# Performance work log

Hardware: AMD Instinct MI355X
Metric: run time of the kernel (lower is better)

## Reference

```python
import jax, jax.numpy as jnp
import numpy as np
from jax import lax

TOP_K = 6
NORM_MIN = 1e-12


def setup_inputs() -> dict:
    key = jax.random.key(0)
    k0, k1, k2, k3, k4, k5 = jax.random.split(key, 6)
    B, S, H, E, I = 2, 1024, 2048, 64, 512
    return {
        "hidden_states": jax.random.normal(k0, (B, S, H), dtype=jnp.float32),
        "gate_w": jax.random.normal(k1, (E, H), dtype=jnp.float32) * 0.02,
        "e_bias": jax.random.normal(k2, (E,), dtype=jnp.float32) * 0.01,
        "gate_proj": jax.random.normal(k3, (E, H, I), dtype=jnp.float32) * 0.02,
        "up_proj": jax.random.normal(k4, (E, H, I), dtype=jnp.float32) * 0.02,
        "down_proj": jax.random.normal(k5, (E, I, H), dtype=jnp.float32) * 0.02,
    }


def reference(hidden_states, gate_w, e_bias, gate_proj, up_proj, down_proj):
    B, S, H = hidden_states.shape
    E = gate_w.shape[0]
    x = hidden_states.reshape(-1, H)                      # [T, H]
    T = x.shape[0]

    # --- routing (done in float32 in the original) ---
    router_logits = x.astype(jnp.float32) @ gate_w.T      # [T, E]
    routing_probs = jax.nn.softmax(router_logits, axis=-1)
    # topk over bias-corrected scores, but weights come from raw probs
    _, selected = lax.top_k(routing_probs + e_bias[None, :], TOP_K)  # [T, k]
    w = jnp.take_along_axis(routing_probs, selected, axis=-1)        # [T, k]
    w = w / jnp.clip(w.sum(axis=-1, keepdims=True), NORM_MIN)
    w = w.astype(hidden_states.dtype)

    # combine weights: [T, E], zero for unselected experts
    combine = jnp.zeros((T, E), dtype=hidden_states.dtype)
    combine = combine.at[jnp.arange(T)[:, None], selected].add(w)

    # --- experts: SwiGLU MLP per expert, weighted-sum combine ---
    def step(acc, params):
        wg, wu, wd, c = params                            # wg,wu [H,I]; wd [I,H]; c [T]
        h = jax.nn.silu(x @ wg) * (x @ wu)                # [T, I]
        return acc + (h @ wd) * c[:, None], None

    init = jnp.zeros((T, H), dtype=hidden_states.dtype)
    final, _ = lax.scan(step, init, (gate_proj, up_proj, down_proj, combine.T))
    return final.reshape(-1), router_logits.reshape(-1)
```

## Files before the change

### kernel.cpp

```cpp
#include <hip/hip_runtime.h>
#include <math.h>

#define T_TOK 2048
#define H_DIM 2048
#define E_NUM 64
#define I_DIM 512
#define TOPK  6
#define NPAIR (T_TOK * TOPK)
#define MAXTILES 80

typedef __attribute__((ext_vector_type(8))) short s8;
typedef __attribute__((ext_vector_type(4))) float f4;
typedef __attribute__((ext_vector_type(8))) unsigned short u16x8;

static __device__ __forceinline__ unsigned short f2bf(float f) {
  unsigned int u = __float_as_uint(f);
  u += 0x7fff + ((u >> 16) & 1);
  return (unsigned short)(u >> 16);
}
static __device__ __forceinline__ unsigned int cvt_pk(float lo, float hi) {
  unsigned int r;
  asm("v_cvt_pk_bf16_f32 %0, %1, %2" : "=v"(r) : "v"(lo), "v"(hi));
  return r;
}
static __device__ __forceinline__ void gload_lds16(const void* g, void* l) {
  __builtin_amdgcn_global_load_lds(
      (const __attribute__((address_space(1))) unsigned int*)g,
      (__attribute__((address_space(3))) unsigned int*)l, 16, 0, 0);
}
#define SBAR()      __builtin_amdgcn_s_barrier()
#define SCHED0()    __builtin_amdgcn_sched_barrier(0)
#define WAIT_LGKM0() asm volatile("s_waitcnt lgkmcnt(0)" ::: "memory")
#define WAIT_VM0()   asm volatile("s_waitcnt vmcnt(0)" ::: "memory")
#define WAIT_VM2()   asm volatile("s_waitcnt vmcnt(2)" ::: "memory")

__global__ __launch_bounds__(256) void router_kernel(
    const float* __restrict__ x, const float* __restrict__ gw,
    const float* __restrict__ ebias, float* __restrict__ logits_out,
    int* __restrict__ sel, float* __restrict__ wsel)
{
  __shared__ float xs[4][H_DIM];
  __shared__ float lg[4][E_NUM];
  int t0 = blockIdx.x * 4;
  int tid = threadIdx.x;
  for (int i = tid; i < 4 * (H_DIM / 4); i += 256) {
    int tt = i >> 9, q = i & 511;
    ((float4*)xs[tt])[q] = ((const float4*)(x + (size_t)(t0 + tt) * H_DIM))[q];
  }
  __syncthreads();

  int wave = tid >> 6, lane = tid & 63;
  for (int ei = 0; ei < 16; ++ei) {
    int e = wave * 16 + ei;
    const float4* gwe = (const float4*)(gw + (size_t)e * H_DIM);
    float s0 = 0.f, s1 = 0.f, s2 = 0.f, s3 = 0.f;
    for (int h4 = lane; h4 < H_DIM / 4; h4 += 64) {
      float4 w4 = gwe[h4];
      float4 a0 = ((const float4*)xs[0])[h4];
      float4 a1 = ((const float4*)xs[1])[h4];
      float4 a2 = ((const float4*)xs[2])[h4];
      float4 a3 = ((const float4*)xs[3])[h4];
      s0 += w4.x*a0.x + w4.y*a0.y + w4.z*a0.z + w4.w*a0.w;
      s1 += w4.x*a1.x + w4.y*a1.y + w4.z*a1.z + w4.w*a1.w;
      s2 += w4.x*a2.x + w4.y*a2.y + w4.z*a2.z + w4.w*a2.w;
      s3 += w4.x*a3.x + w4.y*a3.y + w4.z*a3.z + w4.w*a3.w;
    }
    for (int off = 32; off; off >>= 1) {
      s0 += __shfl_down(s0, off); s1 += __shfl_down(s1, off);
      s2 += __shfl_down(s2, off); s3 += __shfl_down(s3, off);
    }
    if (lane == 0) { lg[0][e] = s0; lg[1][e] = s1; lg[2][e] = s2; lg[3][e] = s3; }
  }
  __syncthreads();

  { int tt = tid >> 6, e = tid & 63;
    logits_out[(size_t)(t0 + tt) * E_NUM + e] = lg[tt][e]; }

  if (wave == 0) {
    for (int tt = 0; tt < 4; ++tt) {
      int t = t0 + tt;
      float v = lg[tt][lane];
      float m = v;
      for (int off = 32; off; off >>= 1) m = fmaxf(m, __shfl_xor(m, off));
      float ex = __expf(v - m);
      float sum = ex;
      for (int off = 32; off; off >>= 1) sum += __shfl_xor(sum, off);
      float prob = ex / sum;
      float sc = prob + ebias[lane];

      int selidx[TOPK]; float selw[TOPK]; float wsum = 0.f;
      #pragma unroll
      for (int k = 0; k < TOPK; ++k) {
        float mm = sc;
        for (int off = 32; off; off >>= 1) mm = fmaxf(mm, __shfl_xor(mm, off));
        unsigned long long ball = __ballot(sc == mm);
        int s = __ffsll(ball) - 1;
        float p = __shfl(prob, s);
        selidx[k] = s; selw[k] = p; wsum += p;
        if (lane == s) sc = -INFINITY;
      }
      if (lane == 0) {
        float inv = 1.f / fmaxf(wsum, 1e-12f);
        #pragma unroll
        for (int k = 0; k < TOPK; ++k) {
          sel[t * TOPK + k] = selidx[k];
          wsel[t * TOPK + k] = selw[k] * inv;
        }
      }
    }
  }
}

__global__ __launch_bounds__(64) void build_lists(
    const int* __restrict__ sel, const float* __restrict__ wsel,
    int* __restrict__ cnt, int* __restrict__ toklist, float* __restrict__ wtlist)
{
  int e = blockIdx.x, lane = threadIdx.x;
  int base = 0;
  for (int t0 = 0; t0 < T_TOK; t0 += 64) {
    int t = t0 + lane;
    int flag = 0; float w = 0.f;
    #pragma unroll
    for (int k = 0; k < TOPK; ++k)
      if (sel[t * TOPK + k] == e) { flag = 1; w = wsel[t * TOPK + k]; }
    unsigned long long b = __ballot(flag);
    int pos = base + __popcll(b & ((1ull << lane) - 1ull));
    if (flag) { toklist[e * T_TOK + pos] = t; wtlist[e * T_TOK + pos] = w; }
    base += __popcll(b);
  }
  if (lane == 0) cnt[e] = base;
}

__global__ void scan_kernel(const int* __restrict__ cnt,
                            int* __restrict__ tmap, int* __restrict__ ntile) {
  if (threadIdx.x == 0) {
    int nt = 0;
    for (int e = 0; e < E_NUM; ++e) {
      int m = (cnt[e] + 255) >> 8;
      for (int tb = 0; tb < m && nt < MAXTILES; ++tb) tmap[nt++] = e * 16 + tb;
    }
    *ntile = nt;
  }
}

__global__ __launch_bounds__(256) void permute_kernel(
    const float* __restrict__ x, const int* __restrict__ cnt,
    const int* __restrict__ toklist, const int* __restrict__ tmap,
    const int* __restrict__ ntile, unsigned short* __restrict__ xt)
{
  int tile = blockIdx.y;
  if (tile >= *ntile) return;
  int ks = blockIdx.x;
  int em = tmap[tile], e = em >> 4, tb = em & 15;
  int n = cnt[e];
  int r = threadIdx.x;
  int tok = toklist[e * T_TOK + min(tb * 256 + r, n - 1)];
  const float4* src = (const float4*)(x + (size_t)tok * H_DIM + ks * 32);
  float4 v[8];
  #pragma unroll
  for (int q = 0; q < 8; ++q) v[q] = src[q];
  int g = (r >> 1) & 3;
  unsigned short* dst = xt + ((size_t)(tile * 64 + ks) * 1024 + r * 4) * 8;
  #pragma unroll
  for (int u = 0; u < 4; ++u) {
    int k16 = u ^ g;
    float4 a = v[2 * k16], b = v[2 * k16 + 1];
    u16x8 p;
    ((unsigned int*)&p)[0] = cvt_pk(a.x, a.y);
    ((unsigned int*)&p)[1] = cvt_pk(a.z, a.w);
    ((unsigned int*)&p)[2] = cvt_pk(b.x, b.y);
    ((unsigned int*)&p)[3] = cvt_pk(b.z, b.w);
    *(u16x8*)(dst + u * 8) = p;
  }
}

__global__ __launch_bounds__(512, 4) void gateup_kernel(
    const unsigned short* __restrict__ xt, const float* __restrict__ gp,
    const float* __restrict__ up, const int* __restrict__ tmap,
    const int* __restrict__ ntile, unsigned short* __restrict__ hat)
{
  __shared__ __align__(16) unsigned short A_lds[2][8192];
  __shared__ __align__(16) unsigned int   Bt[2][2][64 * 20];
  int tile = blockIdx.x;
  if (tile >= *ntile) return;
  int e = tmap[tile] >> 4;
  int ic = blockIdx.y, colbase = ic * 64;
  int tid = threadIdx.x, lane = tid & 63, wave = tid >> 6;
  int matc = wave >> 2, cw = wave & 3;
  int lrow = (lane >> 4) * 4, lcol = lane & 15, kgl = lane >> 4;
  int hp = tid & 15, cb = (tid >> 4) & 15, mstage = tid >> 8;
  const float* bsrc0 = ((mstage == 0) ? gp : up)
      + (size_t)e * (H_DIM * I_DIM) + colbase + (size_t)(2 * hp) * I_DIM + cb * 4;
  const unsigned short* achunk0 = xt + (size_t)tile * 64 * 1024 * 8;

  f4 acc[4][4];
  #pragma unroll
  for (int a = 0; a < 4; ++a)
    #pragma unroll
    for (int b = 0; b < 4; ++b) acc[a][b] = (f4)0.f;

  float4 p0, p1;
  {
    const unsigned short* s = achunk0 + (size_t)(wave * 128 + lane) * 8;
    gload_lds16(s,       &A_lds[0][(wave * 128) * 8]);
    gload_lds16(s + 512, &A_lds[0][(wave * 128 + 64) * 8]);
    p0 = *(const float4*)bsrc0;
    p1 = *(const float4*)(bsrc0 + I_DIM);
    const float* b1 = bsrc0 + (size_t)32 * I_DIM;
    float4 q0 = *(const float4*)b1;
    float4 q1 = *(const float4*)(b1 + I_DIM);
    WAIT_VM2();
    unsigned int* db = &Bt[0][mstage][cb * 4 * 20 + hp];
    db[0]  = cvt_pk(p0.x, p1.x); db[20] = cvt_pk(p0.y, p1.y);
    db[40] = cvt_pk(p0.z, p1.z); db[60] = cvt_pk(p0.w, p1.w);
    p0 = q0; p1 = q1;
    WAIT_LGKM0();
    SBAR();
    SCHED0();
  }

  for (int k = 0; k < 64; ++k) {
    if (k < 63) {
      WAIT_VM0();
      unsigned int* db = &Bt[(k + 1) & 1][mstage][cb * 4 * 20 + hp];
      db[0]  = cvt_pk(p0.x, p1.x); db[20] = cvt_pk(p0.y, p1.y);
      db[40] = cvt_pk(p0.z, p1.z); db[60] = cvt_pk(p0.w, p1.w);
    }
    if (k < 63) {
      const unsigned short* s = achunk0 + ((size_t)(k + 1) * 1024 + wave * 128 + lane) * 8;
      gload_lds16(s,       &A_lds[(k + 1) & 1][(wave * 128) * 8]);
      gload_lds16(s + 512, &A_lds[(k + 1) & 1][(wave * 128 + 64) * 8]);
    }
    if (k < 62) {
      const float* b = bsrc0 + (size_t)(k + 2) * 32 * I_DIM;
      p0 = *(const float4*)b;
      p1 = *(const float4*)(b + I_DIM);
    }
    {
      s8 afr[4];
      #pragma unroll
      for (int mf = 0; mf < 4; ++mf) {
        int r = cw * 64 + mf * 16 + lcol;
        afr[mf] = *(s8*)&A_lds[k & 1][r * 32 + ((kgl ^ ((r >> 1) & 3)) * 8)];
      }
      #pragma unroll
      for (int nf = 0; nf < 4; ++nf) {
        s8 bfr = *(s8*)&Bt[k & 1][matc][(nf * 16 + lcol) * 20 + kgl * 4];
        #pragma unroll
        for (int mf = 0; mf < 4; ++mf)
          acc[mf][nf] = __builtin_amdgcn_mfma_f32_16x16x32_bf16(afr[mf], bfr, acc[mf][nf], 0, 0, 0);
      }
    }
    if (k < 63) {
      WAIT_LGKM0();
      if (k < 62) { WAIT_VM2(); } else { WAIT_VM0(); }
      SBAR();
      SCHED0();
    }
  }

  f4* exch = (f4*)&Bt[0][0][0];
  unsigned short* hs = &A_lds[0][0];
  #pragma unroll
  for (int nf = 0; nf < 4; ++nf) {
    __syncthreads();
    if (wave >= 4) {
      #pragma unroll
      for (int mf = 0; mf < 4; ++mf)
        exch[((wave - 4) * 4 + mf) * 64 + lane] = acc[mf][nf];
    }
    __syncthreads();
    if (wave < 4) {
      #pragma unroll
      for (int mf = 0; mf < 4; ++mf) {
        f4 u = exch[(wave * 4 + mf) * 64 + lane];
        #pragma unroll
        for (int j = 0; j < 4; ++j) {
          float g = acc[mf][nf][j];
          float h = g / (1.f + __expf(-g)) * u[j];
          hs[(wave * 64 + mf * 16 + lrow + j) * 64 + nf * 16 + lcol] = f2bf(h);
        }
      }
    }
  }
  __syncthreads();
  #pragma unroll
  for (int c = 0; c < 2; ++c) {
    unsigned short* base = hat + (size_t)(tile * 16 + ic * 2 + c) * 1024 * 8;
    for (int uu = tid; uu < 1024; uu += 512) {
      int row = uu >> 2, k16 = (uu & 3) ^ ((row >> 1) & 3);
      *(u16x8*)(base + (size_t)uu * 8) = *(const u16x8*)&hs[row * 64 + c * 32 + k16 * 8];
    }
  }
}

__global__ __launch_bounds__(256, 4) void down_kernel(
    const unsigned short* __restrict__ hat, const float* __restrict__ dp,
    const int* __restrict__ cnt, const int* __restrict__ tmap,
    const int* __restrict__ ntile, const int* __restrict__ toklist,
    const float* __restrict__ wtlist, float* __restrict__ out)
{
  __shared__ __align__(16) unsigned short A_lds[2][8192];
  __shared__ __align__(16) unsigned int   Bt[2][64 * 20];
  __shared__ int   stok[256];
  __shared__ float swt[256];
  int tile = blockIdx.x;
  if (tile >= *ntile) return;
  int em = tmap[tile], e = em >> 4, tb = em & 15;
  int n = cnt[e];
  int hc = blockIdx.y, colbase = hc * 64;
  int tid = threadIdx.x, lane = tid & 63, wave = tid >> 6, wbase = wave * 64;
  int lrow = (lane >> 4) * 4, lcol = lane & 15, kgl = lane >> 4;
  int hp = tid & 15, cb = tid >> 4;
  const float* bsrc0 = dp + (size_t)e * (I_DIM * H_DIM) + colbase
                       + (size_t)(2 * hp) * H_DIM + cb * 4;
  const unsigned short* achunk0 = hat + (size_t)tile * 16 * 1024 * 8;

  int rr = tb * 256 + tid;
  stok[tid] = (rr < n) ? toklist[e * T_TOK + rr] : 0;
  swt[tid]  = (rr < n) ? wtlist[e * T_TOK + rr] : 0.f;

  f4 acc[4][4];
  #pragma unroll
  for (int a = 0; a < 4; ++a)
    #pragma unroll
    for (int b = 0; b < 4; ++b) acc[a][b] = (f4)0.f;

  float4 p0, p1;
  {
    const unsigned short* s = achunk0 + (size_t)(wave * 256 + lane) * 8;
    #pragma unroll
    for (int i = 0; i < 4; ++i)
      gload_lds16(s + i * 512, &A_lds[0][(wave * 256 + i * 64) * 8]);
    p0 = *(const float4*)bsrc0;
    p1 = *(const float4*)(bsrc0 + H_DIM);
    const float* b1 = bsrc0 + (size_t)32 * H_DIM;
    float4 q0 = *(const float4*)b1;
    float4 q1 = *(const float4*)(b1 + H_DIM);
    WAIT_VM2();
    unsigned int* db = &Bt[0][cb * 4 * 20 + hp];
    db[0]  = cvt_pk(p0.x, p1.x); db[20] = cvt_pk(p0.y, p1.y);
    db[40] = cvt_pk(p0.z, p1.z); db[60] = cvt_pk(p0.w, p1.w);
    p0 = q0; p1 = q1;
    WAIT_LGKM0();
    SBAR();
    SCHED0();
  }

  for (int k = 0; k < 16; ++k) {
    if (k < 15) {
      WAIT_VM0();
      unsigned int* db = &Bt[(k + 1) & 1][cb * 4 * 20 + hp];
      db[0]  = cvt_pk(p0.x, p1.x); db[20] = cvt_pk(p0.y, p1.y);
      db[40] = cvt_pk(p0.z, p1.z); db[60] = cvt_pk(p0.w, p1.w);
    }
    if (k < 15) {
      const unsigned short* s = achunk0 + ((size_t)(k + 1) * 1024 + wave * 256 + lane) * 8;
      #pragma unroll
      for (int i = 0; i < 4; ++i)
        gload_lds16(s + i * 512, &A_lds[(k + 1) & 1][(wave * 256 + i * 64) * 8]);
    }
    if (k < 14) {
      const float* b = bsrc0 + (size_t)(k + 2) * 32 * H_DIM;
      p0 = *(const float4*)b;
      p1 = *(const float4*)(b + H_DIM);
    }
    {
      s8 afr[4];
      #pragma unroll
      for (int mf = 0; mf < 4; ++mf) {
        int r = wbase + mf * 16 + lcol;
        afr[mf] = *(s8*)&A_lds[k & 1][r * 32 + ((kgl ^ ((r >> 1) & 3)) * 8)];
      }
      #pragma unroll
      for (int nf = 0; nf < 4; ++nf) {
        s8 bfr = *(s8*)&Bt[k & 1][(nf * 16 + lcol) * 20 + kgl * 4];
        #pragma unroll
        for (int mf = 0; mf < 4; ++mf)
          acc[mf][nf] = __builtin_amdgcn_mfma_f32_16x16x32_bf16(afr[mf], bfr, acc[mf][nf], 0, 0, 0);
      }
    }
    if (k < 15) {
      WAIT_LGKM0();
      if (k < 14) { WAIT_VM2(); } else { WAIT_VM0(); }
      SBAR();
      SCHED0();
    }
  }

  __syncthreads();
  #pragma unroll
  for (int mf = 0; mf < 4; ++mf)
    #pragma unroll
    for (int nf = 0; nf < 4; ++nf)
      #pragma unroll
      for (int j = 0; j < 4; ++j) {
        int r = wbase + mf * 16 + lrow + j;
        if (tb * 256 + r < n)
          atomicAdd(&out[(size_t)stok[r] * H_DIM + colbase + nf * 16 + lcol],
                    acc[mf][nf][j] * swt[r]);
      }
}

extern "C" void kernel_launch(void* const* d_in, const int* in_sizes, int n_in,
                              void* d_out, int out_size, void* d_ws, size_t ws_size,
                              hipStream_t stream) {
  const float* hidden = (const float*)d_in[0];
  const float* gate_w = (const float*)d_in[1];
  const float* e_bias = (const float*)d_in[2];
  const float* gate_p = (const float*)d_in[3];
  const float* up_p   = (const float*)d_in[4];
  const float* down_p = (const float*)d_in[5];

  float* out_final  = (float*)d_out;
  float* out_logits = out_final + (size_t)T_TOK * H_DIM;

  int*   cnt     = (int*)d_ws;
  int*   texp    = cnt + 64;
  int*   ntile   = texp + 64;
  int*   tmap    = ntile + 16;
  int*   sel     = tmap + MAXTILES;
  float* wsel    = (float*)(sel + NPAIR);
  int*   toklist = (int*)(wsel + NPAIR);
  float* wtlist  = (float*)(toklist + E_NUM * T_TOK);
  unsigned short* xt  = (unsigned short*)(wtlist + E_NUM * T_TOK);
  unsigned short* hat = xt + (size_t)MAXTILES * 64 * 1024 * 8;

  hipMemsetAsync(out_final, 0, (size_t)T_TOK * H_DIM * sizeof(float), stream);

  router_kernel<<<T_TOK / 4, 256, 0, stream>>>(hidden, gate_w, e_bias, out_logits, sel, wsel);
  build_lists<<<E_NUM, 64, 0, stream>>>(sel, wsel, cnt, toklist, wtlist);
  scan_kernel<<<1, 64, 0, stream>>>(cnt, tmap, ntile);
  permute_kernel<<<dim3(64, MAXTILES), 256, 0, stream>>>(hidden, cnt, toklist, tmap, ntile, xt);
  gateup_kernel<<<dim3(MAXTILES, I_DIM / 64), 512, 0, stream>>>(
      xt, gate_p, up_p, tmap, ntile, hat);
  down_kernel<<<dim3(MAXTILES, H_DIM / 64), 256, 0, stream>>>(
      hat, down_p, cnt, tmap, ntile, toklist, wtlist, out_final);
}
```

Baseline: 610.4 us.

## Triple-buffer A tiles in LDS to prefetch two k-steps ahead

```diff
diff --git a/kernel.cpp b/kernel.cpp
--- a/kernel.cpp
+++ b/kernel.cpp
@@ -32,7 +32,6 @@
 #define SCHED0()    __builtin_amdgcn_sched_barrier(0)
 #define WAIT_LGKM0() asm volatile("s_waitcnt lgkmcnt(0)" ::: "memory")
 #define WAIT_VM0()   asm volatile("s_waitcnt vmcnt(0)" ::: "memory")
-#define WAIT_VM2()   asm volatile("s_waitcnt vmcnt(2)" ::: "memory")
 
 __global__ __launch_bounds__(256) void router_kernel(
     const float* __restrict__ x, const float* __restrict__ gw,
@@ -179,7 +178,7 @@
     const float* __restrict__ up, const int* __restrict__ tmap,
     const int* __restrict__ ntile, unsigned short* __restrict__ hat)
 {
-  __shared__ __align__(16) unsigned short A_lds[2][8192];
+  __shared__ __align__(16) unsigned short A_lds[3][8192];
   __shared__ __align__(16) unsigned int   Bt[2][2][64 * 20];
   int tile = blockIdx.x;
   if (tile >= *ntile) return;
@@ -206,42 +205,44 @@
     gload_lds16(s + 512, &A_lds[0][(wave * 128 + 64) * 8]);
     p0 = *(const float4*)bsrc0;
     p1 = *(const float4*)(bsrc0 + I_DIM);
-    const float* b1 = bsrc0 + (size_t)32 * I_DIM;
-    float4 q0 = *(const float4*)b1;
-    float4 q1 = *(const float4*)(b1 + I_DIM);
-    WAIT_VM2();
+    WAIT_VM0();
     unsigned int* db = &Bt[0][mstage][cb * 4 * 20 + hp];
     db[0]  = cvt_pk(p0.x, p1.x); db[20] = cvt_pk(p0.y, p1.y);
     db[40] = cvt_pk(p0.z, p1.z); db[60] = cvt_pk(p0.w, p1.w);
-    p0 = q0; p1 = q1;
+    const unsigned short* s1 = achunk0 + (size_t)(1024 + wave * 128 + lane) * 8;
+    gload_lds16(s1,       &A_lds[1][(wave * 128) * 8]);
+    gload_lds16(s1 + 512, &A_lds[1][(wave * 128 + 64) * 8]);
+    const float* b1 = bsrc0 + (size_t)32 * I_DIM;
+    p0 = *(const float4*)b1;
+    p1 = *(const float4*)(b1 + I_DIM);
     WAIT_LGKM0();
     SBAR();
     SCHED0();
   }
 
   for (int k = 0; k < 64; ++k) {
-    if (k < 63) {
+    if (k + 1 < 64) {
       WAIT_VM0();
       unsigned int* db = &Bt[(k + 1) & 1][mstage][cb * 4 * 20 + hp];
       db[0]  = cvt_pk(p0.x, p1.x); db[20] = cvt_pk(p0.y, p1.y);
       db[40] = cvt_pk(p0.z, p1.z); db[60] = cvt_pk(p0.w, p1.w);
     }
-    if (k < 63) {
-      const unsigned short* s = achunk0 + ((size_t)(k + 1) * 1024 + wave * 128 + lane) * 8;
-      gload_lds16(s,       &A_lds[(k + 1) & 1][(wave * 128) * 8]);
-      gload_lds16(s + 512, &A_lds[(k + 1) & 1][(wave * 128 + 64) * 8]);
-    }
-    if (k < 62) {
+    if (k + 2 < 64) {
+      int ab = (k + 2) % 3;
+      const unsigned short* s = achunk0 + ((size_t)(k + 2) * 1024 + wave * 128 + lane) * 8;
+      gload_lds16(s,       &A_lds[ab][(wave * 128) * 8]);
+      gload_lds16(s + 512, &A_lds[ab][(wave * 128 + 64) * 8]);
       const float* b = bsrc0 + (size_t)(k + 2) * 32 * I_DIM;
       p0 = *(const float4*)b;
       p1 = *(const float4*)(b + I_DIM);
     }
     {
+      int ab = k % 3;
       s8 afr[4];
       #pragma unroll
       for (int mf = 0; mf < 4; ++mf) {
         int r = cw * 64 + mf * 16 + lcol;
-        afr[mf] = *(s8*)&A_lds[k & 1][r * 32 + ((kgl ^ ((r >> 1) & 3)) * 8)];
+        afr[mf] = *(s8*)&A_lds[ab][r * 32 + ((kgl ^ ((r >> 1) & 3)) * 8)];
       }
       #pragma unroll
       for (int nf = 0; nf < 4; ++nf) {
@@ -251,12 +252,9 @@
           acc[mf][nf] = __builtin_amdgcn_mfma_f32_16x16x32_bf16(afr[mf], bfr, acc[mf][nf], 0, 0, 0);
       }
     }
-    if (k < 63) {
-      WAIT_LGKM0();
-      if (k < 62) { WAIT_VM2(); } else { WAIT_VM0(); }
-      SBAR();
-      SCHED0();
-    }
+    WAIT_LGKM0();
+    SBAR();
+    SCHED0();
   }
 
   f4* exch = (f4*)&Bt[0][0][0];
@@ -300,7 +298,7 @@
     const int* __restrict__ ntile, const int* __restrict__ toklist,
     const float* __restrict__ wtlist, float* __restrict__ out)
 {
-  __shared__ __align__(16) unsigned short A_lds[2][8192];
+  __shared__ __align__(16) unsigned short A_lds[3][8192];
   __shared__ __align__(16) unsigned int   Bt[2][64 * 20];
   __shared__ int   stok[256];
   __shared__ float swt[256];
@@ -334,43 +332,46 @@
       gload_lds16(s + i * 512, &A_lds[0][(wave * 256 + i * 64) * 8]);
     p0 = *(const float4*)bsrc0;
     p1 = *(const float4*)(bsrc0 + H_DIM);
-    const float* b1 = bsrc0 + (size_t)32 * H_DIM;
-    float4 q0 = *(const float4*)b1;
-    float4 q1 = *(const float4*)(b1 + H_DIM);
-    WAIT_VM2();
+    WAIT_VM0();
     unsigned int* db = &Bt[0][cb * 4 * 20 + hp];
     db[0]  = cvt_pk(p0.x, p1.x); db[20] = cvt_pk(p0.y, p1.y);
     db[40] = cvt_pk(p0.z, p1.z); db[60] = cvt_pk(p0.w, p1.w);
-    p0 = q0; p1 = q1;
+    const unsigned short* s1 = achunk0 + (size_t)(1024 + wave * 256 + lane) * 8;
+    #pragma unroll
+    for (int i = 0; i < 4; ++i)
+      gload_lds16(s1 + i * 512, &A_lds[1][(wave * 256 + i * 64) * 8]);
+    const float* b1 = bsrc0 + (size_t)32 * H_DIM;
+    p0 = *(const float4*)b1;
+    p1 = *(const float4*)(b1 + H_DIM);
     WAIT_LGKM0();
     SBAR();
     SCHED0();
   }
 
   for (int k = 0; k < 16; ++k) {
-    if (k < 15) {
+    if (k + 1 < 16) {
       WAIT_VM0();
       unsigned int* db = &Bt[(k + 1) & 1][cb * 4 * 20 + hp];
       db[0]  = cvt_pk(p0.x, p1.x); db[20] = cvt_pk(p0.y, p1.y);
       db[40] = cvt_pk(p0.z, p1.z); db[60] = cvt_pk(p0.w, p1.w);
     }
-    if (k < 15) {
-      const unsigned short* s = achunk0 + ((size_t)(k + 1) * 1024 + wave * 256 + lane) * 8;
+    if (k + 2 < 16) {
+      int ab = (k + 2) % 3;
+      const unsigned short* s = achunk0 + ((size_t)(k + 2) * 1024 + wave * 256 + lane) * 8;
       #pragma unroll
       for (int i = 0; i < 4; ++i)
-        gload_lds16(s + i * 512, &A_lds[(k + 1) & 1][(wave * 256 + i * 64) * 8]);
-    }
-    if (k < 14) {
+        gload_lds16(s + i * 512, &A_lds[ab][(wave * 256 + i * 64) * 8]);
       const float* b = bsrc0 + (size_t)(k + 2) * 32 * H_DIM;
       p0 = *(const float4*)b;
       p1 = *(const float4*)(b + H_DIM);
     }
     {
+      int ab = k % 3;
       s8 afr[4];
       #pragma unroll
       for (int mf = 0; mf < 4; ++mf) {
         int r = wbase + mf * 16 + lcol;
-        afr[mf] = *(s8*)&A_lds[k & 1][r * 32 + ((kgl ^ ((r >> 1) & 3)) * 8)];
+        afr[mf] = *(s8*)&A_lds[ab][r * 32 + ((kgl ^ ((r >> 1) & 3)) * 8)];
       }
       #pragma unroll
       for (int nf = 0; nf < 4; ++nf) {
@@ -380,15 +381,11 @@
           acc[mf][nf] = __builtin_amdgcn_mfma_f32_16x16x32_bf16(afr[mf], bfr, acc[mf][nf], 0, 0, 0);
       }
     }
-    if (k < 15) {
-      WAIT_LGKM0();
-      if (k < 14) { WAIT_VM2(); } else { WAIT_VM0(); }
-      SBAR();
-      SCHED0();
-    }
-  }
-
-  __syncthreads();
+    WAIT_LGKM0();
+    SBAR();
+    SCHED0();
+  }
+
   #pragma unroll
   for (int mf = 0; mf < 4; ++mf)
     #pragma unroll
```

Result: no change. 610.1 us (-0.1%).
